# Kernel tuning notes

Hardware: AMD Instinct MI355X
Metric: run time of the kernel (lower is better)

## Reference

```python
import jax, jax.numpy as jnp
import numpy as np

T, B, H, L = 64, 128, 256, 2  # steps/stack_size, batch, hidden, layers


def setup_inputs() -> dict:
    key = jax.random.key(0)
    ks = jax.random.split(key, 6)
    s = 1.0 / np.sqrt(H)
    x = jax.random.normal(ks[0], (T, B, H), dtype=jnp.float32)
    ops = jax.random.randint(ks[1], (T, B), 0, 2, dtype=jnp.int32)  # push=1, hold=0
    W_ih = jax.random.uniform(ks[2], (L, 4 * H, H), jnp.float32, -s, s)
    W_hh = jax.random.uniform(ks[3], (L, 4 * H, H), jnp.float32, -s, s)
    b_ih = jax.random.uniform(ks[4], (L, 4 * H), jnp.float32, -s, s)
    b_hh = jax.random.uniform(ks[5], (L, 4 * H), jnp.float32, -s, s)
    return {"x": x, "ops": ops, "W_ih": W_ih, "W_hh": W_hh, "b_ih": b_ih, "b_hh": b_hh}


def reference(x, ops, W_ih, W_hh, b_ih, b_hh):
    T_, B_, H_ = x.shape
    L_ = W_ih.shape[0]
    bidx = jnp.arange(B_)

    def cell(xt, h_prev, c_prev):
        # multi-layer LSTM cell; layer l>0 takes layer l-1 hidden as input (dropout=0)
        inp = xt
        hs, cs = [], []
        for l in range(L_):
            gates = inp @ W_ih[l].T + b_ih[l] + h_prev[..., l] @ W_hh[l].T + b_hh[l]
            i, f, g, o = jnp.split(gates, 4, axis=-1)
            c = jax.nn.sigmoid(f) * c_prev[..., l] + jax.nn.sigmoid(i) * jnp.tanh(g)
            h = jax.nn.sigmoid(o) * jnp.tanh(c)
            hs.append(h)
            cs.append(c)
            inp = h
        return jnp.stack(hs, axis=-1), jnp.stack(cs, axis=-1)  # (B, H, L)

    def step(carry, xt_op):
        hstack, cstack, pos = carry  # stacks: (T+1, B, H, L), pos: (B,)
        xt, opt = xt_op
        h_prev = hstack[pos, bidx]  # gather top-of-stack, (B, H, L)
        c_prev = cstack[pos, bidx]
        nh, nc = cell(xt, h_prev, c_prev)
        # hold_or_push writes at pos+1 for every batch element, then pos += op
        hstack = hstack.at[pos + 1, bidx].set(nh)
        cstack = cstack.at[pos + 1, bidx].set(nc)
        pos = pos + opt
        return (hstack, cstack, pos), nh[..., -1]  # last-layer hidden output

    hs0 = jnp.zeros((T_ + 1, B_, H_, L_), dtype=x.dtype)
    cs0 = jnp.zeros((T_ + 1, B_, H_, L_), dtype=x.dtype)
    pos0 = jnp.zeros((B_,), dtype=jnp.int32)
    _, outs = jax.lax.scan(step, (hs0, cs0, pos0), (x, ops))
    return outs  # (T, B, H)
```

## Files before the change

### kernel.cpp

```cpp
#include <hip/hip_runtime.h>
#include <hip/hip_fp16.h>
#include <cstddef>

#define TT 64
#define BB 128
#define HH 256
#define G4 1024
#define BLK 256
#define NBG 32

#define OFF_HX0 0u
#define OFF_HX1 65536u
#define OFF_XG  131072u

__device__ __forceinline__ float sigf(float x) { return 1.0f / (1.0f + expf(-x)); }

typedef _Float16 h2v __attribute__((ext_vector_type(2)));

__device__ __forceinline__ float dot2acc(unsigned w, unsigned h, float acc) {
#if __has_builtin(__builtin_amdgcn_fdot2)
  return __builtin_amdgcn_fdot2(__builtin_bit_cast(h2v, w),
                                __builtin_bit_cast(h2v, h), acc, false);
#else
  __half2 wv = *(__half2*)&w, hv = *(__half2*)&h;
  float2 wf = __half22float2(wv), hf = __half22float2(hv);
  return fmaf(wf.x, hf.x, fmaf(wf.y, hf.y, acc));
#endif
}

__device__ __forceinline__ unsigned packh2(float e, float o) {
  return (unsigned)__half_as_ushort(__float2half(e)) |
         ((unsigned)__half_as_ushort(__float2half(o)) << 16);
}

__device__ __forceinline__ int hsw(int b, int k2) {
  return b * 144 + k2 + ((k2 >> 5) << 2);
}

__global__ void __launch_bounds__(256, 2)
xg_gemm(const float* __restrict__ X,
        const float* __restrict__ W,
        const float* __restrict__ bias,
        float* __restrict__ ws) {
  float* __restrict__ Xg = ws + OFF_XG;
  const int m0 = blockIdx.x * 128;
  const int n0 = blockIdx.y * 128;
  const int tid = threadIdx.x;
  const int tx = tid & 15, ty = tid >> 4;

  __shared__ __align__(16) float Xs[64][132];
  __shared__ __align__(16) float Wn[64][132];

  const int lr = tid >> 1, lk = (tid & 1) * 32;
  const float* xrow = X + (size_t)(m0 + lr) * HH + lk;
  const float* wrow = W + (size_t)(n0 + lr) * HH + lk;

  float acc[8][8];
#pragma unroll
  for (int i = 0; i < 8; ++i)
#pragma unroll
    for (int j = 0; j < 8; ++j) acc[i][j] = 0.f;

  for (int ks = 0; ks < 4; ++ks) {
    {
      const float* xp = xrow + ks * 64;
      const float* wp = wrow + ks * 64;
      float4 v[4];
#pragma unroll
      for (int q = 0; q < 4; ++q) v[q] = *(const float4*)(xp + q * 4);
#pragma unroll
      for (int q = 0; q < 4; ++q) {
        Xs[lk + q * 4 + 0][lr] = v[q].x;
        Xs[lk + q * 4 + 1][lr] = v[q].y;
        Xs[lk + q * 4 + 2][lr] = v[q].z;
        Xs[lk + q * 4 + 3][lr] = v[q].w;
      }
#pragma unroll
      for (int q = 0; q < 4; ++q) v[q] = *(const float4*)(xp + 16 + q * 4);
#pragma unroll
      for (int q = 0; q < 4; ++q) {
        Xs[lk + 16 + q * 4 + 0][lr] = v[q].x;
        Xs[lk + 16 + q * 4 + 1][lr] = v[q].y;
        Xs[lk + 16 + q * 4 + 2][lr] = v[q].z;
        Xs[lk + 16 + q * 4 + 3][lr] = v[q].w;
      }
#pragma unroll
      for (int q = 0; q < 4; ++q) v[q] = *(const float4*)(wp + q * 4);
#pragma unroll
      for (int q = 0; q < 4; ++q) {
        Wn[lk + q * 4 + 0][lr] = v[q].x;
        Wn[lk + q * 4 + 1][lr] = v[q].y;
        Wn[lk + q * 4 + 2][lr] = v[q].z;
        Wn[lk + q * 4 + 3][lr] = v[q].w;
      }
#pragma unroll
      for (int q = 0; q < 4; ++q) v[q] = *(const float4*)(wp + 16 + q * 4);
#pragma unroll
      for (int q = 0; q < 4; ++q) {
        Wn[lk + 16 + q * 4 + 0][lr] = v[q].x;
        Wn[lk + 16 + q * 4 + 1][lr] = v[q].y;
        Wn[lk + 16 + q * 4 + 2][lr] = v[q].z;
        Wn[lk + 16 + q * 4 + 3][lr] = v[q].w;
      }
    }
    __syncthreads();

#pragma unroll 8
    for (int k = 0; k < 64; ++k) {
      const float4 a0 = *(const float4*)&Xs[k][ty * 8];
      const float4 a1 = *(const float4*)&Xs[k][ty * 8 + 4];
      const float4 b0 = *(const float4*)&Wn[k][tx * 4];
      const float4 b1 = *(const float4*)&Wn[k][64 + tx * 4];
      const float ar[8] = {a0.x, a0.y, a0.z, a0.w, a1.x, a1.y, a1.z, a1.w};
      const float br[8] = {b0.x, b0.y, b0.z, b0.w, b1.x, b1.y, b1.z, b1.w};
#pragma unroll
      for (int i = 0; i < 8; ++i)
#pragma unroll
        for (int j = 0; j < 8; ++j) acc[i][j] = fmaf(ar[i], br[j], acc[i][j]);
    }
    __syncthreads();
  }

  const int t = m0 >> 7;
#pragma unroll
  for (int h = 0; h < 2; ++h) {
    const int base = n0 + h * 64 + tx * 4;
    const int hg = (base >> 4) & 15;
    const int lc = ((base >> 8) << 4) | (base & 15);
    const float4 bv = *(const float4*)(bias + base);
#pragma unroll
    for (int i = 0; i < 8; ++i) {
      const int b = ty * 8 + i;
      float4 v;
      v.x = acc[i][h * 4 + 0] + bv.x;
      v.y = acc[i][h * 4 + 1] + bv.y;
      v.z = acc[i][h * 4 + 2] + bv.z;
      v.w = acc[i][h * 4 + 3] + bv.w;
      *(float4*)&Xg[(((size_t)t * 16 + hg) * 128 + b) * 64 + lc] = v;
    }
  }
}

__global__ void __launch_bounds__(BLK, 2)
seq9(const float* __restrict__ W_ih,
     const float* __restrict__ W_hh,
     const float* __restrict__ b_ih,
     const float* __restrict__ b_hh,
     const int* __restrict__ ops,
     float* __restrict__ ws,
     float* __restrict__ out) {
  const int bg = blockIdx.x & 31;
  const int hg = blockIdx.x >> 5;
  const int tid = threadIdx.x;
  const int kq = tid & 7;
  const int c2 = tid >> 3;

  __shared__ __align__(16) float XgL[TT * 256];
  __shared__ __align__(16) unsigned hp0[4 * 144];
  __shared__ __align__(16) unsigned hp1[4 * 144];
  __shared__ __align__(16) unsigned h0c[4 * 144];
  __shared__ float gatA[256];
  __shared__ float gatB[256];
  __shared__ int opsA[TT * 4];

  unsigned wr0[32], wr1[32], wr2[32];
  {
    const float* s0 = W_hh;
    const float* s1 = W_ih + (size_t)G4 * HH;
    const float* s2 = W_hh + (size_t)G4 * HH;
#pragma unroll
    for (int j = 0; j < 2; ++j) {
      const int lc = c2 * 2 + j;
      const int g = ((lc >> 4) << 8) + hg * 16 + (lc & 15);
      const float* p0 = s0 + (size_t)g * HH + kq * 32;
      const float* p1 = s1 + (size_t)g * HH + kq * 32;
      const float* p2 = s2 + (size_t)g * HH + kq * 32;
#pragma unroll
      for (int i = 0; i < 16; ++i) {
        wr0[j * 16 + i] = packh2(p0[2 * i], p0[2 * i + 1]);
        wr1[j * 16 + i] = packh2(p1[2 * i], p1[2 * i + 1]);
        wr2[j * 16 + i] = packh2(p2[2 * i], p2[2 * i + 1]);
      }
    }
  }
  float bias0r[2], bias1r[2];
#pragma unroll
  for (int j = 0; j < 2; ++j) {
    const int lc = c2 * 2 + j;
    const int g = ((lc >> 4) << 8) + hg * 16 + (lc & 15);
    bias0r[j] = b_hh[g];
    bias1r[j] = b_ih[G4 + g] + b_hh[G4 + g];
  }
  for (int i = tid; i < TT * 64; i += BLK) {
    const int t = i >> 6, r = i & 63;
    ((float4*)XgL)[i] = *(const float4*)(
        ws + OFF_XG + (((size_t)t * 16 + hg) * 128 + bg * 4) * 64 + r * 4);
  }
  for (int i = tid; i < TT * 4; i += BLK)
    opsA[i] = ops[(i >> 2) * BB + bg * 4 + (i & 3)];
  for (int i = tid; i < 4 * 144; i += BLK) { hp0[i] = 0u; hp1[i] = 0u; }

  unsigned long long* __restrict__ Hx0 = (unsigned long long*)(ws + OFF_HX0);
  unsigned long long* __restrict__ Hx1 = (unsigned long long*)(ws + OFF_HX1);
  float cp0 = 0.f, cp1 = 0.f;
  float a0r[4][2] = {{0.f, 0.f}, {0.f, 0.f}, {0.f, 0.f}, {0.f, 0.f}};
  float a1q[4][2] = {{0.f, 0.f}, {0.f, 0.f}, {0.f, 0.f}, {0.f, 0.f}};
  __syncthreads();

  for (int t = 0; t < TT; ++t) {
    const int par = t & 1;

#pragma unroll
    for (int b = 0; b < 4; ++b) {
      if (t > 0 && opsA[(t - 1) * 4 + b]) {
        const unsigned* hb = &hp0[b * 144 + kq * 16 + ((kq >> 1) << 2)];
        const uint4 x0 = *(const uint4*)(hb + 0);
        const uint4 x1 = *(const uint4*)(hb + 4);
        const uint4 x2 = *(const uint4*)(hb + 8);
        const uint4 x3 = *(const uint4*)(hb + 12);
        const unsigned hh[16] = {x0.x, x0.y, x0.z, x0.w, x1.x, x1.y, x1.z, x1.w,
                                 x2.x, x2.y, x2.z, x2.w, x3.x, x3.y, x3.z, x3.w};
        float s0 = 0.f, s1 = 0.f;
#pragma unroll
        for (int i = 0; i < 16; ++i) {
          s0 = dot2acc(wr0[i], hh[i], s0);
          s1 = dot2acc(wr0[16 + i], hh[i], s1);
        }
#pragma unroll
        for (int m = 1; m <= 4; m <<= 1) {
          s0 += __shfl_xor(s0, m, 64);
          s1 += __shfl_xor(s1, m, 64);
        }
        a0r[b][0] = s0;
        a0r[b][1] = s1;
      }
    }
    if (kq == 0) {
#pragma unroll
      for (int b = 0; b < 4; ++b)
        *(float2*)&gatA[b * 64 + c2 * 2] =
            make_float2(a0r[b][0] + bias0r[0], a0r[b][1] + bias0r[1]);
    }
    __syncthreads();

    if (tid < 64) {
      const int b = tid >> 4, r = tid & 15;
      const float* xg = &XgL[t * 256 + b * 64];
      const float* gt = &gatA[b * 64];
      const float ig = gt[r] + xg[r],           fg = gt[16 + r] + xg[16 + r];
      const float gg = gt[32 + r] + xg[32 + r], og = gt[48 + r] + xg[48 + r];
      const float c = sigf(fg) * cp0 + sigf(ig) * tanhf(gg);
      const float h = sigf(og) * tanhf(c);
      if (opsA[t * 4 + b]) cp0 = c;
      const float ho = __shfl_xor(h, 1, 64);
      if (!(r & 1)) {
        const unsigned long long v =
            (unsigned long long)(unsigned)(t + 1) |
            ((unsigned long long)packh2(h, ho) << 32);
        __hip_atomic_store(
            Hx0 + ((size_t)par * NBG + bg) * 512 + b * 128 + hg * 8 + (r >> 1),
            v, __ATOMIC_RELAXED, __HIP_MEMORY_SCOPE_AGENT);
      }
    }

    {
      const unsigned long long* s0 = Hx0 + ((size_t)par * NBG + bg) * 512;
      const unsigned long long* s1 = Hx1 + ((size_t)(par ^ 1) * NBG + bg) * 512;
      const unsigned tagA = (unsigned)(t + 1);
      const unsigned tagB = (unsigned)t;
      const int idx1 = tid + 256;
      const int b0 = tid >> 7, k20 = tid & 127;
      const int b1 = idx1 >> 7, k21 = idx1 & 127;
      const bool need1a = (t > 0) && (opsA[(t - 1) * 4 + b0] != 0);
      const bool need1b = (t > 0) && (opsA[(t - 1) * 4 + b1] != 0);
      unsigned long long v0 = 0, v1 = 0, w0 = 0, w1 = 0;
      bool d0 = false, d1 = false, e0 = !need1a, e1 = !need1b;
      int spins = 0;
      for (;;) {
        if (!d0) v0 = __hip_atomic_load(s0 + tid, __ATOMIC_RELAXED,
                                        __HIP_MEMORY_SCOPE_AGENT);
        if (!d1) v1 = __hip_atomic_load(s0 + idx1, __ATOMIC_RELAXED,
                                        __HIP_MEMORY_SCOPE_AGENT);
        if (!e0) w0 = __hip_atomic_load(s1 + tid, __ATOMIC_RELAXED,
                                        __HIP_MEMORY_SCOPE_AGENT);
        if (!e1) w1 = __hip_atomic_load(s1 + idx1, __ATOMIC_RELAXED,
                                        __HIP_MEMORY_SCOPE_AGENT);
        d0 = d0 || ((unsigned)v0 == tagA);
        d1 = d1 || ((unsigned)v1 == tagA);
        e0 = e0 || ((unsigned)w0 == tagB);
        e1 = e1 || ((unsigned)w1 == tagB);
        if (d0 && d1 && e0 && e1) break;
        if (++spins > (1 << 18)) break;
        if (spins > 2) __builtin_amdgcn_s_sleep(1);
      }
      const unsigned p0 = (unsigned)(v0 >> 32), p1 = (unsigned)(v1 >> 32);
      const int sw0 = hsw(b0, k20), sw1 = hsw(b1, k21);
      h0c[sw0] = p0;
      h0c[sw1] = p1;
      if (opsA[t * 4 + b0]) hp0[sw0] = p0;
      if (opsA[t * 4 + b1]) hp0[sw1] = p1;
      if (need1a) hp1[sw0] = (unsigned)(w0 >> 32);
      if (need1b) hp1[sw1] = (unsigned)(w1 >> 32);
    }
    __syncthreads();

    float fr[4][2];
#pragma unroll
    for (int b = 0; b < 4; ++b) {
      const unsigned* cb = &h0c[b * 144 + kq * 16 + ((kq >> 1) << 2)];
      const uint4 c0 = *(const uint4*)(cb + 0);
      const uint4 c1 = *(const uint4*)(cb + 4);
      const uint4 c2v = *(const uint4*)(cb + 8);
      const uint4 c3 = *(const uint4*)(cb + 12);
      const unsigned hc[16] = {c0.x, c0.y, c0.z, c0.w, c1.x, c1.y, c1.z, c1.w,
                               c2v.x, c2v.y, c2v.z, c2v.w, c3.x, c3.y, c3.z, c3.w};
      float s0 = 0.f, s1 = 0.f;
#pragma unroll
      for (int i = 0; i < 16; ++i) {
        s0 = dot2acc(wr1[i], hc[i], s0);
        s1 = dot2acc(wr1[16 + i], hc[i], s1);
      }
      if (t > 0 && opsA[(t - 1) * 4 + b]) {
        const unsigned* qb = &hp1[b * 144 + kq * 16 + ((kq >> 1) << 2)];
        const uint4 q0 = *(const uint4*)(qb + 0);
        const uint4 q1 = *(const uint4*)(qb + 4);
        const uint4 q2 = *(const uint4*)(qb + 8);
        const uint4 q3 = *(const uint4*)(qb + 12);
        const unsigned hq[16] = {q0.x, q0.y, q0.z, q0.w, q1.x, q1.y, q1.z, q1.w,
                                 q2.x, q2.y, q2.z, q2.w, q3.x, q3.y, q3.z, q3.w};
        float t0 = 0.f, t1 = 0.f;
#pragma unroll
        for (int i = 0; i < 16; ++i) {
          t0 = dot2acc(wr2[i], hq[i], t0);
          t1 = dot2acc(wr2[16 + i], hq[i], t1);
        }
#pragma unroll
        for (int m = 1; m <= 4; m <<= 1) {
          t0 += __shfl_xor(t0, m, 64);
          t1 += __shfl_xor(t1, m, 64);
        }
        a1q[b][0] = t0;
        a1q[b][1] = t1;
      }
#pragma unroll
      for (int m = 1; m <= 4; m <<= 1) {
        s0 += __shfl_xor(s0, m, 64);
        s1 += __shfl_xor(s1, m, 64);
      }
      fr[b][0] = s0;
      fr[b][1] = s1;
    }
    if (kq == 0) {
#pragma unroll
      for (int b = 0; b < 4; ++b)
        *(float2*)&gatB[b * 64 + c2 * 2] =
            make_float2(fr[b][0] + a1q[b][0] + bias1r[0],
                        fr[b][1] + a1q[b][1] + bias1r[1]);
    }
    __syncthreads();

    if (tid < 64) {
      const int b = tid >> 4, r = tid & 15;
      const float* gt = &gatB[b * 64];
      const float ig = gt[r],      fg = gt[16 + r];
      const float gg = gt[32 + r], og = gt[48 + r];
      const float c = sigf(fg) * cp1 + sigf(ig) * tanhf(gg);
      const float h = sigf(og) * tanhf(c);
      const int op = opsA[t * 4 + b];
      if (op) cp1 = c;
      out[((size_t)t * BB + bg * 4 + b) * HH + hg * 16 + r] = h;
      const float ho = __shfl_xor(h, 1, 64);
      if (op && !(r & 1)) {
        const unsigned long long v =
            (unsigned long long)(unsigned)(t + 1) |
            ((unsigned long long)packh2(h, ho) << 32);
        __hip_atomic_store(
            Hx1 + ((size_t)par * NBG + bg) * 512 + b * 128 + hg * 8 + (r >> 1),
            v, __ATOMIC_RELAXED, __HIP_MEMORY_SCOPE_AGENT);
      }
    }
  }
}

extern "C" void kernel_launch(void* const* d_in, const int* in_sizes, int n_in,
                              void* d_out, int out_size, void* d_ws, size_t ws_size,
                              hipStream_t stream) {
  const float* x    = (const float*)d_in[0];
  const int*   ops  = (const int*)d_in[1];
  const float* W_ih = (const float*)d_in[2];
  const float* W_hh = (const float*)d_in[3];
  const float* b_ih = (const float*)d_in[4];
  const float* b_hh = (const float*)d_in[5];
  float* out = (float*)d_out;
  float* ws  = (float*)d_ws;

  xg_gemm<<<dim3(64, 8), 256, 0, stream>>>(x, W_ih, b_ih, ws);
  seq9<<<512, BLK, 0, stream>>>(W_ih, W_hh, b_ih, b_hh, ops, ws, out);
}
```

Before: 487.5 us.

## Repartition LSTM recurrence to 512-thread blocks over 2 batches and 32 hidden units

The persistent recurrent kernel now gives each block 2 batch rows and 32 hidden units instead of 4 and 16, using 512 threads. Per-thread register weight slices stay the same size, but each block covers more gate columns with fewer batch rows, and the Xg workspace layout is reshaped to match. The spin-wait is also split so that half the threads poll the layer-0 flags and the other half poll the layer-1 flags independently. The aim is to cut per-thread serial work per step and shorten polling, at the cost of larger blocks and more register pressure at 4 waves per SIMD.

```diff
diff --git a/kernel.cpp b/kernel.cpp
--- a/kernel.cpp
+++ b/kernel.cpp
@@ -6,8 +6,9 @@
 #define BB 128
 #define HH 256
 #define G4 1024
-#define BLK 256
-#define NBG 32
+#define BLK 512
+#define NBG 64
+#define NHG 8
 
 #define OFF_HX0 0u
 #define OFF_HX1 65536u
@@ -125,8 +126,8 @@
 #pragma unroll
   for (int h = 0; h < 2; ++h) {
     const int base = n0 + h * 64 + tx * 4;
-    const int hg = (base >> 4) & 15;
-    const int lc = ((base >> 8) << 4) | (base & 15);
+    const int hg = (base >> 5) & 7;
+    const int lc = ((base >> 8) << 5) | (base & 31);
     const float4 bv = *(const float4*)(bias + base);
 #pragma unroll
     for (int i = 0; i < 8; ++i) {
@@ -136,34 +137,35 @@
       v.y = acc[i][h * 4 + 1] + bv.y;
       v.z = acc[i][h * 4 + 2] + bv.z;
       v.w = acc[i][h * 4 + 3] + bv.w;
-      *(float4*)&Xg[(((size_t)t * 16 + hg) * 128 + b) * 64 + lc] = v;
-    }
-  }
-}
-
-__global__ void __launch_bounds__(BLK, 2)
-seq9(const float* __restrict__ W_ih,
-     const float* __restrict__ W_hh,
-     const float* __restrict__ b_ih,
-     const float* __restrict__ b_hh,
-     const int* __restrict__ ops,
-     float* __restrict__ ws,
-     float* __restrict__ out) {
-  const int bg = blockIdx.x & 31;
-  const int hg = blockIdx.x >> 5;
+      *(float4*)&Xg[(((size_t)t * NHG + hg) * 128 + b) * 128 + lc] = v;
+    }
+  }
+}
+
+__global__ void __launch_bounds__(BLK, 4)
+seq18(const float* __restrict__ W_ih,
+      const float* __restrict__ W_hh,
+      const float* __restrict__ b_ih,
+      const float* __restrict__ b_hh,
+      const int* __restrict__ ops,
+      float* __restrict__ ws,
+      float* __restrict__ out) {
+  const int bg = blockIdx.x & 63;
+  const int hg = blockIdx.x >> 6;
   const int tid = threadIdx.x;
   const int kq = tid & 7;
   const int c2 = tid >> 3;
 
   __shared__ __align__(16) float XgL[TT * 256];
-  __shared__ __align__(16) unsigned hp0[4 * 144];
-  __shared__ __align__(16) unsigned hp1[4 * 144];
-  __shared__ __align__(16) unsigned h0c[4 * 144];
+  __shared__ __align__(16) unsigned hp0[2 * 144];
+  __shared__ __align__(16) unsigned hp1[2 * 144];
+  __shared__ __align__(16) unsigned h0c[2 * 144];
   __shared__ float gatA[256];
   __shared__ float gatB[256];
-  __shared__ int opsA[TT * 4];
+  __shared__ int opsA[TT * 2];
 
   unsigned wr0[32], wr1[32], wr2[32];
+  float bias0r[2], bias1r[2];
   {
     const float* s0 = W_hh;
     const float* s1 = W_ih + (size_t)G4 * HH;
@@ -171,7 +173,7 @@
 #pragma unroll
     for (int j = 0; j < 2; ++j) {
       const int lc = c2 * 2 + j;
-      const int g = ((lc >> 4) << 8) + hg * 16 + (lc & 15);
+      const int g = ((lc >> 5) << 8) + hg * 32 + (lc & 31);
       const float* p0 = s0 + (size_t)g * HH + kq * 32;
       const float* p1 = s1 + (size_t)g * HH + kq * 32;
       const float* p2 = s2 + (size_t)g * HH + kq * 32;
@@ -181,38 +183,31 @@
         wr1[j * 16 + i] = packh2(p1[2 * i], p1[2 * i + 1]);
         wr2[j * 16 + i] = packh2(p2[2 * i], p2[2 * i + 1]);
       }
-    }
-  }
-  float bias0r[2], bias1r[2];
-#pragma unroll
-  for (int j = 0; j < 2; ++j) {
-    const int lc = c2 * 2 + j;
-    const int g = ((lc >> 4) << 8) + hg * 16 + (lc & 15);
-    bias0r[j] = b_hh[g];
-    bias1r[j] = b_ih[G4 + g] + b_hh[G4 + g];
+      bias0r[j] = b_hh[g];
+      bias1r[j] = b_ih[G4 + g] + b_hh[G4 + g];
+    }
   }
   for (int i = tid; i < TT * 64; i += BLK) {
-    const int t = i >> 6, r = i & 63;
+    const int t = i >> 6, rem = i & 63, b = rem >> 5, l4 = rem & 31;
     ((float4*)XgL)[i] = *(const float4*)(
-        ws + OFF_XG + (((size_t)t * 16 + hg) * 128 + bg * 4) * 64 + r * 4);
-  }
-  for (int i = tid; i < TT * 4; i += BLK)
-    opsA[i] = ops[(i >> 2) * BB + bg * 4 + (i & 3)];
-  for (int i = tid; i < 4 * 144; i += BLK) { hp0[i] = 0u; hp1[i] = 0u; }
+        ws + OFF_XG + (((size_t)t * NHG + hg) * 128 + bg * 2 + b) * 128 + l4 * 4);
+  }
+  if (tid < TT * 2) opsA[tid] = ops[(tid >> 1) * BB + bg * 2 + (tid & 1)];
+  if (tid < 2 * 144) { hp0[tid] = 0u; hp1[tid] = 0u; }
 
   unsigned long long* __restrict__ Hx0 = (unsigned long long*)(ws + OFF_HX0);
   unsigned long long* __restrict__ Hx1 = (unsigned long long*)(ws + OFF_HX1);
   float cp0 = 0.f, cp1 = 0.f;
-  float a0r[4][2] = {{0.f, 0.f}, {0.f, 0.f}, {0.f, 0.f}, {0.f, 0.f}};
-  float a1q[4][2] = {{0.f, 0.f}, {0.f, 0.f}, {0.f, 0.f}, {0.f, 0.f}};
+  float a0r[2][2] = {{0.f, 0.f}, {0.f, 0.f}};
+  float a1q[2][2] = {{0.f, 0.f}, {0.f, 0.f}};
   __syncthreads();
 
   for (int t = 0; t < TT; ++t) {
     const int par = t & 1;
 
 #pragma unroll
-    for (int b = 0; b < 4; ++b) {
-      if (t > 0 && opsA[(t - 1) * 4 + b]) {
+    for (int b = 0; b < 2; ++b) {
+      if (t > 0 && opsA[(t - 1) * 2 + b]) {
         const unsigned* hb = &hp0[b * 144 + kq * 16 + ((kq >> 1) << 2)];
         const uint4 x0 = *(const uint4*)(hb + 0);
         const uint4 x1 = *(const uint4*)(hb + 4);
@@ -237,76 +232,72 @@
     }
     if (kq == 0) {
 #pragma unroll
-      for (int b = 0; b < 4; ++b)
-        *(float2*)&gatA[b * 64 + c2 * 2] =
+      for (int b = 0; b < 2; ++b)
+        *(float2*)&gatA[b * 128 + c2 * 2] =
             make_float2(a0r[b][0] + bias0r[0], a0r[b][1] + bias0r[1]);
     }
     __syncthreads();
 
     if (tid < 64) {
-      const int b = tid >> 4, r = tid & 15;
-      const float* xg = &XgL[t * 256 + b * 64];
-      const float* gt = &gatA[b * 64];
-      const float ig = gt[r] + xg[r],           fg = gt[16 + r] + xg[16 + r];
-      const float gg = gt[32 + r] + xg[32 + r], og = gt[48 + r] + xg[48 + r];
+      const int b = tid >> 5, r = tid & 31;
+      const float* xg = &XgL[t * 256 + b * 128];
+      const float* gt = &gatA[b * 128];
+      const float ig = gt[r] + xg[r],           fg = gt[32 + r] + xg[32 + r];
+      const float gg = gt[64 + r] + xg[64 + r], og = gt[96 + r] + xg[96 + r];
       const float c = sigf(fg) * cp0 + sigf(ig) * tanhf(gg);
       const float h = sigf(og) * tanhf(c);
-      if (opsA[t * 4 + b]) cp0 = c;
+      if (opsA[t * 2 + b]) cp0 = c;
       const float ho = __shfl_xor(h, 1, 64);
       if (!(r & 1)) {
         const unsigned long long v =
             (unsigned long long)(unsigned)(t + 1) |
             ((unsigned long long)packh2(h, ho) << 32);
         __hip_atomic_store(
-            Hx0 + ((size_t)par * NBG + bg) * 512 + b * 128 + hg * 8 + (r >> 1),
+            Hx0 + ((size_t)par * NBG + bg) * 256 + b * 128 + hg * 16 + (r >> 1),
             v, __ATOMIC_RELAXED, __HIP_MEMORY_SCOPE_AGENT);
       }
     }
 
-    {
-      const unsigned long long* s0 = Hx0 + ((size_t)par * NBG + bg) * 512;
-      const unsigned long long* s1 = Hx1 + ((size_t)(par ^ 1) * NBG + bg) * 512;
+    if (tid < 256) {
+      const unsigned long long* s0 = Hx0 + ((size_t)par * NBG + bg) * 256;
       const unsigned tagA = (unsigned)(t + 1);
-      const unsigned tagB = (unsigned)t;
-      const int idx1 = tid + 256;
       const int b0 = tid >> 7, k20 = tid & 127;
-      const int b1 = idx1 >> 7, k21 = idx1 & 127;
-      const bool need1a = (t > 0) && (opsA[(t - 1) * 4 + b0] != 0);
-      const bool need1b = (t > 0) && (opsA[(t - 1) * 4 + b1] != 0);
-      unsigned long long v0 = 0, v1 = 0, w0 = 0, w1 = 0;
-      bool d0 = false, d1 = false, e0 = !need1a, e1 = !need1b;
+      unsigned long long v = __hip_atomic_load(s0 + tid, __ATOMIC_RELAXED,
+                                               __HIP_MEMORY_SCOPE_AGENT);
       int spins = 0;
-      for (;;) {
-        if (!d0) v0 = __hip_atomic_load(s0 + tid, __ATOMIC_RELAXED,
-                                        __HIP_MEMORY_SCOPE_AGENT);
-        if (!d1) v1 = __hip_atomic_load(s0 + idx1, __ATOMIC_RELAXED,
-                                        __HIP_MEMORY_SCOPE_AGENT);
-        if (!e0) w0 = __hip_atomic_load(s1 + tid, __ATOMIC_RELAXED,
-                                        __HIP_MEMORY_SCOPE_AGENT);
-        if (!e1) w1 = __hip_atomic_load(s1 + idx1, __ATOMIC_RELAXED,
-                                        __HIP_MEMORY_SCOPE_AGENT);
-        d0 = d0 || ((unsigned)v0 == tagA);
-        d1 = d1 || ((unsigned)v1 == tagA);
-        e0 = e0 || ((unsigned)w0 == tagB);
-        e1 = e1 || ((unsigned)w1 == tagB);
-        if (d0 && d1 && e0 && e1) break;
+      while ((unsigned)v != tagA) {
         if (++spins > (1 << 18)) break;
         if (spins > 2) __builtin_amdgcn_s_sleep(1);
-      }
-      const unsigned p0 = (unsigned)(v0 >> 32), p1 = (unsigned)(v1 >> 32);
-      const int sw0 = hsw(b0, k20), sw1 = hsw(b1, k21);
-      h0c[sw0] = p0;
-      h0c[sw1] = p1;
-      if (opsA[t * 4 + b0]) hp0[sw0] = p0;
-      if (opsA[t * 4 + b1]) hp0[sw1] = p1;
-      if (need1a) hp1[sw0] = (unsigned)(w0 >> 32);
-      if (need1b) hp1[sw1] = (unsigned)(w1 >> 32);
-    }
-    __syncthreads();
-
-    float fr[4][2];
-#pragma unroll
-    for (int b = 0; b < 4; ++b) {
+        v = __hip_atomic_load(s0 + tid, __ATOMIC_RELAXED,
+                              __HIP_MEMORY_SCOPE_AGENT);
+      }
+      const unsigned p = (unsigned)(v >> 32);
+      const int sw = hsw(b0, k20);
+      h0c[sw] = p;
+      if (opsA[t * 2 + b0]) hp0[sw] = p;
+    } else {
+      const int u = tid - 256;
+      const int b1 = u >> 7, k21 = u & 127;
+      if (t > 0 && opsA[(t - 1) * 2 + b1]) {
+        const unsigned long long* s1 = Hx1 + ((size_t)(par ^ 1) * NBG + bg) * 256;
+        const unsigned tagB = (unsigned)t;
+        unsigned long long w = __hip_atomic_load(s1 + u, __ATOMIC_RELAXED,
+                                                 __HIP_MEMORY_SCOPE_AGENT);
+        int spins = 0;
+        while ((unsigned)w != tagB) {
+          if (++spins > (1 << 18)) break;
+          if (spins > 2) __builtin_amdgcn_s_sleep(1);
+          w = __hip_atomic_load(s1 + u, __ATOMIC_RELAXED,
+                                __HIP_MEMORY_SCOPE_AGENT);
+        }
+        hp1[hsw(b1, k21)] = (unsigned)(w >> 32);
+      }
+    }
+    __syncthreads();
+
+    float fr[2][2];
+#pragma unroll
+    for (int b = 0; b < 2; ++b) {
       const unsigned* cb = &h0c[b * 144 + kq * 16 + ((kq >> 1) << 2)];
       const uint4 c0 = *(const uint4*)(cb + 0);
       const uint4 c1 = *(const uint4*)(cb + 4);
@@ -320,7 +311,7 @@
         s0 = dot2acc(wr1[i], hc[i], s0);
         s1 = dot2acc(wr1[16 + i], hc[i], s1);
       }
-      if (t > 0 && opsA[(t - 1) * 4 + b]) {
+      if (t > 0 && opsA[(t - 1) * 2 + b]) {
         const unsigned* qb = &hp1[b * 144 + kq * 16 + ((kq >> 1) << 2)];
         const uint4 q0 = *(const uint4*)(qb + 0);
         const uint4 q1 = *(const uint4*)(qb + 4);
@@ -352,30 +343,30 @@
     }
     if (kq == 0) {
 #pragma unroll
-      for (int b = 0; b < 4; ++b)
-        *(float2*)&gatB[b * 64 + c2 * 2] =
+      for (int b = 0; b < 2; ++b)
+        *(float2*)&gatB[b * 128 + c2 * 2] =
             make_float2(fr[b][0] + a1q[b][0] + bias1r[0],
                         fr[b][1] + a1q[b][1] + bias1r[1]);
     }
     __syncthreads();
 
     if (tid < 64) {
-      const int b = tid >> 4, r = tid & 15;
-      const float* gt = &gatB[b * 64];
-      const float ig = gt[r],      fg = gt[16 + r];
-      const float gg = gt[32 + r], og = gt[48 + r];
+      const int b = tid >> 5, r = tid & 31;
+      const float* gt = &gatB[b * 128];
+      const float ig = gt[r],      fg = gt[32 + r];
+      const float gg = gt[64 + r], og = gt[96 + r];
       const float c = sigf(fg) * cp1 + sigf(ig) * tanhf(gg);
       const float h = sigf(og) * tanhf(c);
-      const int op = opsA[t * 4 + b];
+      const int op = opsA[t * 2 + b];
       if (op) cp1 = c;
-      out[((size_t)t * BB + bg * 4 + b) * HH + hg * 16 + r] = h;
+      out[((size_t)t * BB + bg * 2 + b) * HH + hg * 32 + r] = h;
       const float ho = __shfl_xor(h, 1, 64);
       if (op && !(r & 1)) {
         const unsigned long long v =
             (unsigned long long)(unsigned)(t + 1) |
             ((unsigned long long)packh2(h, ho) << 32);
         __hip_atomic_store(
-            Hx1 + ((size_t)par * NBG + bg) * 512 + b * 128 + hg * 8 + (r >> 1),
+            Hx1 + ((size_t)par * NBG + bg) * 256 + b * 128 + hg * 16 + (r >> 1),
             v, __ATOMIC_RELAXED, __HIP_MEMORY_SCOPE_AGENT);
       }
     }
@@ -395,5 +386,5 @@
   float* ws  = (float*)d_ws;
 
   xg_gemm<<<dim3(64, 8), 256, 0, stream>>>(x, W_ih, b_ih, ws);
-  seq9<<<512, BLK, 0, stream>>>(W_ih, W_hh, b_ih, b_hh, ops, ws, out);
-}
+  seq18<<<512, BLK, 0, stream>>>(W_ih, W_hh, b_ih, b_hh, ops, ws, out);
+}
```

Result: slower. 987.7 us (+102.6%).

## Software-pipeline layer 0 and layer 1 across timesteps in persistent LSTM kernel

Applied to the files above, without the earlier changes.

Restructures the time loop so each iteration does one cross-block exchange, then computes layer-0 gates for step t and layer-1 gates for step t-1 together. The layer-1 elementwise update runs on a second wavefront in parallel with the layer-0 update. This removes one global spin-wait and one barrier phase per step from the serial chain. In exchange it adds an extra epilogue iteration and more complex tag and parity bookkeeping.

```diff
diff --git a/kernel.cpp b/kernel.cpp
--- a/kernel.cpp
+++ b/kernel.cpp
@@ -142,13 +142,13 @@
 }
 
 __global__ void __launch_bounds__(BLK, 2)
-seq9(const float* __restrict__ W_ih,
-     const float* __restrict__ W_hh,
-     const float* __restrict__ b_ih,
-     const float* __restrict__ b_hh,
-     const int* __restrict__ ops,
-     float* __restrict__ ws,
-     float* __restrict__ out) {
+seq19(const float* __restrict__ W_ih,
+      const float* __restrict__ W_hh,
+      const float* __restrict__ b_ih,
+      const float* __restrict__ b_hh,
+      const int* __restrict__ ops,
+      float* __restrict__ ws,
+      float* __restrict__ out) {
   const int bg = blockIdx.x & 31;
   const int hg = blockIdx.x >> 5;
   const int tid = threadIdx.x;
@@ -202,77 +202,25 @@
 
   unsigned long long* __restrict__ Hx0 = (unsigned long long*)(ws + OFF_HX0);
   unsigned long long* __restrict__ Hx1 = (unsigned long long*)(ws + OFF_HX1);
-  float cp0 = 0.f, cp1 = 0.f;
+  float cp0 = 0.f;
+  float cp1 = 0.f;
   float a0r[4][2] = {{0.f, 0.f}, {0.f, 0.f}, {0.f, 0.f}, {0.f, 0.f}};
   float a1q[4][2] = {{0.f, 0.f}, {0.f, 0.f}, {0.f, 0.f}, {0.f, 0.f}};
   __syncthreads();
 
-  for (int t = 0; t < TT; ++t) {
-    const int par = t & 1;
-
-#pragma unroll
-    for (int b = 0; b < 4; ++b) {
-      if (t > 0 && opsA[(t - 1) * 4 + b]) {
-        const unsigned* hb = &hp0[b * 144 + kq * 16 + ((kq >> 1) << 2)];
-        const uint4 x0 = *(const uint4*)(hb + 0);
-        const uint4 x1 = *(const uint4*)(hb + 4);
-        const uint4 x2 = *(const uint4*)(hb + 8);
-        const uint4 x3 = *(const uint4*)(hb + 12);
-        const unsigned hh[16] = {x0.x, x0.y, x0.z, x0.w, x1.x, x1.y, x1.z, x1.w,
-                                 x2.x, x2.y, x2.z, x2.w, x3.x, x3.y, x3.z, x3.w};
-        float s0 = 0.f, s1 = 0.f;
-#pragma unroll
-        for (int i = 0; i < 16; ++i) {
-          s0 = dot2acc(wr0[i], hh[i], s0);
-          s1 = dot2acc(wr0[16 + i], hh[i], s1);
-        }
-#pragma unroll
-        for (int m = 1; m <= 4; m <<= 1) {
-          s0 += __shfl_xor(s0, m, 64);
-          s1 += __shfl_xor(s1, m, 64);
-        }
-        a0r[b][0] = s0;
-        a0r[b][1] = s1;
-      }
-    }
-    if (kq == 0) {
-#pragma unroll
-      for (int b = 0; b < 4; ++b)
-        *(float2*)&gatA[b * 64 + c2 * 2] =
-            make_float2(a0r[b][0] + bias0r[0], a0r[b][1] + bias0r[1]);
-    }
-    __syncthreads();
-
-    if (tid < 64) {
-      const int b = tid >> 4, r = tid & 15;
-      const float* xg = &XgL[t * 256 + b * 64];
-      const float* gt = &gatA[b * 64];
-      const float ig = gt[r] + xg[r],           fg = gt[16 + r] + xg[16 + r];
-      const float gg = gt[32 + r] + xg[32 + r], og = gt[48 + r] + xg[48 + r];
-      const float c = sigf(fg) * cp0 + sigf(ig) * tanhf(gg);
-      const float h = sigf(og) * tanhf(c);
-      if (opsA[t * 4 + b]) cp0 = c;
-      const float ho = __shfl_xor(h, 1, 64);
-      if (!(r & 1)) {
-        const unsigned long long v =
-            (unsigned long long)(unsigned)(t + 1) |
-            ((unsigned long long)packh2(h, ho) << 32);
-        __hip_atomic_store(
-            Hx0 + ((size_t)par * NBG + bg) * 512 + b * 128 + hg * 8 + (r >> 1),
-            v, __ATOMIC_RELAXED, __HIP_MEMORY_SCOPE_AGENT);
-      }
-    }
-
-    {
-      const unsigned long long* s0 = Hx0 + ((size_t)par * NBG + bg) * 512;
-      const unsigned long long* s1 = Hx1 + ((size_t)(par ^ 1) * NBG + bg) * 512;
-      const unsigned tagA = (unsigned)(t + 1);
-      const unsigned tagB = (unsigned)t;
+  for (int t = 0; t <= TT; ++t) {
+    if (t >= 1) {
+      const unsigned long long* s0 =
+          Hx0 + ((size_t)((t - 1) & 1) * NBG + bg) * 512;
+      const unsigned long long* s1 =
+          Hx1 + ((size_t)((t >= 2 ? t - 2 : 0) & 1) * NBG + bg) * 512;
+      const unsigned tagA = (unsigned)t;
+      const unsigned tagB = (unsigned)(t - 1);
       const int idx1 = tid + 256;
       const int b0 = tid >> 7, k20 = tid & 127;
       const int b1 = idx1 >> 7, k21 = idx1 & 127;
-      const bool need1a = (t > 0) && (opsA[(t - 1) * 4 + b0] != 0);
-      const bool need1b = (t > 0) && (opsA[(t - 1) * 4 + b1] != 0);
+      const bool need1a = (t >= 2) && (opsA[(t - 2) * 4 + b0] != 0);
+      const bool need1b = (t >= 2) && (opsA[(t - 2) * 4 + b1] != 0);
       unsigned long long v0 = 0, v1 = 0, w0 = 0, w1 = 0;
       bool d0 = false, d1 = false, e0 = !need1a, e1 = !need1b;
       int spins = 0;
@@ -297,85 +245,136 @@
       const int sw0 = hsw(b0, k20), sw1 = hsw(b1, k21);
       h0c[sw0] = p0;
       h0c[sw1] = p1;
-      if (opsA[t * 4 + b0]) hp0[sw0] = p0;
-      if (opsA[t * 4 + b1]) hp0[sw1] = p1;
+      if (opsA[(t - 1) * 4 + b0]) hp0[sw0] = p0;
+      if (opsA[(t - 1) * 4 + b1]) hp0[sw1] = p1;
       if (need1a) hp1[sw0] = (unsigned)(w0 >> 32);
       if (need1b) hp1[sw1] = (unsigned)(w1 >> 32);
     }
     __syncthreads();
 
-    float fr[4][2];
-#pragma unroll
-    for (int b = 0; b < 4; ++b) {
-      const unsigned* cb = &h0c[b * 144 + kq * 16 + ((kq >> 1) << 2)];
-      const uint4 c0 = *(const uint4*)(cb + 0);
-      const uint4 c1 = *(const uint4*)(cb + 4);
-      const uint4 c2v = *(const uint4*)(cb + 8);
-      const uint4 c3 = *(const uint4*)(cb + 12);
-      const unsigned hc[16] = {c0.x, c0.y, c0.z, c0.w, c1.x, c1.y, c1.z, c1.w,
-                               c2v.x, c2v.y, c2v.z, c2v.w, c3.x, c3.y, c3.z, c3.w};
-      float s0 = 0.f, s1 = 0.f;
-#pragma unroll
-      for (int i = 0; i < 16; ++i) {
-        s0 = dot2acc(wr1[i], hc[i], s0);
-        s1 = dot2acc(wr1[16 + i], hc[i], s1);
-      }
-      if (t > 0 && opsA[(t - 1) * 4 + b]) {
-        const unsigned* qb = &hp1[b * 144 + kq * 16 + ((kq >> 1) << 2)];
-        const uint4 q0 = *(const uint4*)(qb + 0);
-        const uint4 q1 = *(const uint4*)(qb + 4);
-        const uint4 q2 = *(const uint4*)(qb + 8);
-        const uint4 q3 = *(const uint4*)(qb + 12);
-        const unsigned hq[16] = {q0.x, q0.y, q0.z, q0.w, q1.x, q1.y, q1.z, q1.w,
-                                 q2.x, q2.y, q2.z, q2.w, q3.x, q3.y, q3.z, q3.w};
-        float t0 = 0.f, t1 = 0.f;
+    if (t < TT) {
+#pragma unroll
+      for (int b = 0; b < 4; ++b) {
+        if (t >= 1 && opsA[(t - 1) * 4 + b]) {
+          const unsigned* hb = &hp0[b * 144 + kq * 16 + ((kq >> 1) << 2)];
+          const uint4 x0 = *(const uint4*)(hb + 0);
+          const uint4 x1 = *(const uint4*)(hb + 4);
+          const uint4 x2 = *(const uint4*)(hb + 8);
+          const uint4 x3 = *(const uint4*)(hb + 12);
+          const unsigned hh[16] = {x0.x, x0.y, x0.z, x0.w, x1.x, x1.y, x1.z, x1.w,
+                                   x2.x, x2.y, x2.z, x2.w, x3.x, x3.y, x3.z, x3.w};
+          float s0 = 0.f, s1 = 0.f;
+#pragma unroll
+          for (int i = 0; i < 16; ++i) {
+            s0 = dot2acc(wr0[i], hh[i], s0);
+            s1 = dot2acc(wr0[16 + i], hh[i], s1);
+          }
+#pragma unroll
+          for (int m = 1; m <= 4; m <<= 1) {
+            s0 += __shfl_xor(s0, m, 64);
+            s1 += __shfl_xor(s1, m, 64);
+          }
+          a0r[b][0] = s0;
+          a0r[b][1] = s1;
+        }
+      }
+      if (kq == 0) {
+#pragma unroll
+        for (int b = 0; b < 4; ++b)
+          *(float2*)&gatA[b * 64 + c2 * 2] =
+              make_float2(a0r[b][0] + bias0r[0], a0r[b][1] + bias0r[1]);
+      }
+    }
+    if (t >= 1) {
+#pragma unroll
+      for (int b = 0; b < 4; ++b) {
+        const unsigned* cb = &h0c[b * 144 + kq * 16 + ((kq >> 1) << 2)];
+        const uint4 c0 = *(const uint4*)(cb + 0);
+        const uint4 c1 = *(const uint4*)(cb + 4);
+        const uint4 c2v = *(const uint4*)(cb + 8);
+        const uint4 c3 = *(const uint4*)(cb + 12);
+        const unsigned hc[16] = {c0.x, c0.y, c0.z, c0.w, c1.x, c1.y, c1.z, c1.w,
+                                 c2v.x, c2v.y, c2v.z, c2v.w, c3.x, c3.y, c3.z, c3.w};
+        float s0 = 0.f, s1 = 0.f;
 #pragma unroll
         for (int i = 0; i < 16; ++i) {
-          t0 = dot2acc(wr2[i], hq[i], t0);
-          t1 = dot2acc(wr2[16 + i], hq[i], t1);
+          s0 = dot2acc(wr1[i], hc[i], s0);
+          s1 = dot2acc(wr1[16 + i], hc[i], s1);
+        }
+        if (t >= 2 && opsA[(t - 2) * 4 + b]) {
+          const unsigned* qb = &hp1[b * 144 + kq * 16 + ((kq >> 1) << 2)];
+          const uint4 q0 = *(const uint4*)(qb + 0);
+          const uint4 q1 = *(const uint4*)(qb + 4);
+          const uint4 q2 = *(const uint4*)(qb + 8);
+          const uint4 q3 = *(const uint4*)(qb + 12);
+          const unsigned hq[16] = {q0.x, q0.y, q0.z, q0.w, q1.x, q1.y, q1.z, q1.w,
+                                   q2.x, q2.y, q2.z, q2.w, q3.x, q3.y, q3.z, q3.w};
+          float t0 = 0.f, t1 = 0.f;
+#pragma unroll
+          for (int i = 0; i < 16; ++i) {
+            t0 = dot2acc(wr2[i], hq[i], t0);
+            t1 = dot2acc(wr2[16 + i], hq[i], t1);
+          }
+#pragma unroll
+          for (int m = 1; m <= 4; m <<= 1) {
+            t0 += __shfl_xor(t0, m, 64);
+            t1 += __shfl_xor(t1, m, 64);
+          }
+          a1q[b][0] = t0;
+          a1q[b][1] = t1;
         }
 #pragma unroll
         for (int m = 1; m <= 4; m <<= 1) {
-          t0 += __shfl_xor(t0, m, 64);
-          t1 += __shfl_xor(t1, m, 64);
-        }
-        a1q[b][0] = t0;
-        a1q[b][1] = t1;
-      }
-#pragma unroll
-      for (int m = 1; m <= 4; m <<= 1) {
-        s0 += __shfl_xor(s0, m, 64);
-        s1 += __shfl_xor(s1, m, 64);
-      }
-      fr[b][0] = s0;
-      fr[b][1] = s1;
-    }
-    if (kq == 0) {
-#pragma unroll
-      for (int b = 0; b < 4; ++b)
-        *(float2*)&gatB[b * 64 + c2 * 2] =
-            make_float2(fr[b][0] + a1q[b][0] + bias1r[0],
-                        fr[b][1] + a1q[b][1] + bias1r[1]);
+          s0 += __shfl_xor(s0, m, 64);
+          s1 += __shfl_xor(s1, m, 64);
+        }
+        if (kq == 0)
+          *(float2*)&gatB[b * 64 + c2 * 2] =
+              make_float2(s0 + a1q[b][0] + bias1r[0],
+                          s1 + a1q[b][1] + bias1r[1]);
+      }
     }
     __syncthreads();
 
     if (tid < 64) {
-      const int b = tid >> 4, r = tid & 15;
+      if (t < TT) {
+        const int b = tid >> 4, r = tid & 15;
+        const float* xg = &XgL[t * 256 + b * 64];
+        const float* gt = &gatA[b * 64];
+        const float ig = gt[r] + xg[r],           fg = gt[16 + r] + xg[16 + r];
+        const float gg = gt[32 + r] + xg[32 + r], og = gt[48 + r] + xg[48 + r];
+        const float c = sigf(fg) * cp0 + sigf(ig) * tanhf(gg);
+        const float h = sigf(og) * tanhf(c);
+        if (opsA[t * 4 + b]) cp0 = c;
+        const float ho = __shfl_xor(h, 1, 64);
+        if (!(r & 1)) {
+          const unsigned long long v =
+              (unsigned long long)(unsigned)(t + 1) |
+              ((unsigned long long)packh2(h, ho) << 32);
+          __hip_atomic_store(
+              Hx0 + ((size_t)(t & 1) * NBG + bg) * 512 + b * 128 + hg * 8 + (r >> 1),
+              v, __ATOMIC_RELAXED, __HIP_MEMORY_SCOPE_AGENT);
+        }
+      }
+    } else if (tid < 128 && t >= 1) {
+      const int s = t - 1;
+      const int u = tid - 64;
+      const int b = u >> 4, r = u & 15;
       const float* gt = &gatB[b * 64];
       const float ig = gt[r],      fg = gt[16 + r];
       const float gg = gt[32 + r], og = gt[48 + r];
       const float c = sigf(fg) * cp1 + sigf(ig) * tanhf(gg);
       const float h = sigf(og) * tanhf(c);
-      const int op = opsA[t * 4 + b];
+      const int op = opsA[s * 4 + b];
       if (op) cp1 = c;
-      out[((size_t)t * BB + bg * 4 + b) * HH + hg * 16 + r] = h;
+      out[((size_t)s * BB + bg * 4 + b) * HH + hg * 16 + r] = h;
       const float ho = __shfl_xor(h, 1, 64);
       if (op && !(r & 1)) {
         const unsigned long long v =
-            (unsigned long long)(unsigned)(t + 1) |
+            (unsigned long long)(unsigned)(s + 1) |
             ((unsigned long long)packh2(h, ho) << 32);
         __hip_atomic_store(
-            Hx1 + ((size_t)par * NBG + bg) * 512 + b * 128 + hg * 8 + (r >> 1),
+            Hx1 + ((size_t)(s & 1) * NBG + bg) * 512 + b * 128 + hg * 8 + (r >> 1),
             v, __ATOMIC_RELAXED, __HIP_MEMORY_SCOPE_AGENT);
       }
     }
@@ -395,5 +394,5 @@
   float* ws  = (float*)d_ws;
 
   xg_gemm<<<dim3(64, 8), 256, 0, stream>>>(x, W_ih, b_ih, ws);
-  seq9<<<512, BLK, 0, stream>>>(W_ih, W_hh, b_ih, b_hh, ops, ws, out);
-}
+  seq19<<<512, BLK, 0, stream>>>(W_ih, W_hh, b_ih, b_hh, ops, ws, out);
+}
```

Result: slower. 502.5 us (+3.1%).
